# Performance work log

Hardware: AMD Instinct MI355X
Metric: run time of the kernel (lower is better)

## Reference

```python
import jax, jax.numpy as jnp
import numpy as np


def _conv1x1(w, b, x):
    # 1x1 Conv2d == channel matmul: w [O,C], x [B,C,H,W] -> [B,O,H,W]
    return jnp.einsum('oc,bchw->bohw', w, x) + b[None, :, None, None]


def setup_inputs() -> dict:
    key = jax.random.key(0)
    ks = jax.random.split(key, 9)
    C = 512
    B, H, W = 8, 32, 32
    s = 0.02
    return {
        'x': jax.random.normal(ks[0], (B, C, H, W), dtype=jnp.float32),
        'wq': jax.random.normal(ks[1], (C, C), dtype=jnp.float32) * s,
        'bq': jax.random.normal(ks[2], (C,), dtype=jnp.float32) * s,
        'wk': jax.random.normal(ks[3], (C, C), dtype=jnp.float32) * s,
        'bk': jax.random.normal(ks[4], (C,), dtype=jnp.float32) * s,
        'wv': jax.random.normal(ks[5], (C, C), dtype=jnp.float32) * s,
        'bv': jax.random.normal(ks[6], (C,), dtype=jnp.float32) * s,
        'wo': jax.random.normal(ks[7], (C, C), dtype=jnp.float32) * s,
        'bo': jax.random.normal(ks[8], (C,), dtype=jnp.float32) * s,
        'heads': 8,
    }


def reference(x, wq, bq, wk, bk, wv, bv, wo, bo, heads):
    B, C, H, W = x.shape
    N = H * W
    d = C // heads
    scale = jnp.asarray(d, x.dtype) ** 0.5

    vx = _conv1x1(wv, bv, x)                       # value(x), reused for residual
    Q = _conv1x1(wq, bq, x).reshape(B, heads, d, N)
    K = _conv1x1(wk, bk, x).reshape(B, heads, d, N)
    V = vx.reshape(B, heads, d, N)

    attn = jax.nn.softmax(jnp.einsum('bhcn,bhcm->bhnm', Q, K) / scale, axis=-1)
    attn_out = jnp.einsum('bhnm,bhcm->bhcn', attn, V).reshape(B, C, H, W)

    out = attn_out + vx                            # residual uses value(x)
    return _conv1x1(wo, bo, out)
```

## Files before the change

### kernel.cpp

```cpp
#include <hip/hip_runtime.h>
#include <cstdint>
#include <cmath>

#define B_ 8
#define C_ 512
#define N_ 1024
#define H_ 8
#define D_ 64


using u16 = unsigned short;

typedef __bf16 bf16x8 __attribute__((ext_vector_type(8)));
typedef float  f32x4  __attribute__((ext_vector_type(4)));
typedef unsigned short us8 __attribute__((ext_vector_type(8)));


__device__ __forceinline__ float b2f(u16 u) {
    return __uint_as_float(((uint32_t)u) << 16);
}
__device__ __forceinline__ u16 f2b(float f) {
    uint32_t x = __float_as_uint(f);
    return (u16)((x + 0x7fffu + ((x >> 16) & 1u)) >> 16);
}
__device__ __forceinline__ u16 f2bt(float f) {
    return (u16)(__float_as_uint(f) >> 16);
}
__device__ __forceinline__ float sf(float f) {
    return (fabsf(f) < 1e30f) ? f : 0.0f;
}
__device__ __forceinline__ u16 sf2b(float f) { return f2b(sf(f)); }

template<bool WB>
__device__ __forceinline__ us8 ldw(const void* W, size_t idx) {
    if constexpr (WB) {
        return *(const us8*)((const u16*)W + idx);
    } else {
        const float* p = (const float*)W + idx;
        float4 a = *(const float4*)p, b = *(const float4*)(p + 4);
        us8 pk;
        pk[0] = sf2b(a.x); pk[1] = sf2b(a.y); pk[2] = sf2b(a.z); pk[3] = sf2b(a.w);
        pk[4] = sf2b(b.x); pk[5] = sf2b(b.y); pk[6] = sf2b(b.z); pk[7] = sf2b(b.w);
        return pk;
    }
}


__global__ __launch_bounds__(256) void k_wconv(
    const float* __restrict__ wq, const float* __restrict__ wk,
    const float* __restrict__ wv, const float* __restrict__ wo,
    u16* __restrict__ wb) {
    int i = blockIdx.x * 256 + threadIdx.x;
    int m = i >> 16;
    int off = (i & 65535) << 2;
    const float* src = (m == 0) ? wq : (m == 1) ? wk : (m == 2) ? wv : wo;
    float4 v = *(const float4*)&src[off];
    ushort4 w;
    w.x = sf2b(v.x); w.y = sf2b(v.y); w.z = sf2b(v.z); w.w = sf2b(v.w);
    *(ushort4*)&wb[(m << 18) + off] = w;
}


__global__ __launch_bounds__(256) void k_transpose(const float* __restrict__ x,
                                                   u16* __restrict__ xt) {
    __shared__ __align__(16) u16 t[64][72];
    const int tid = threadIdx.x;
    const int nb = blockIdx.x, cb = blockIdx.y, b = blockIdx.z;
#pragma unroll
    for (int i = 0; i < 4; ++i) {
        int q = tid + i * 256;
        int row = q >> 4, cg = q & 15;
        float4 v = *(const float4*)&x[((size_t)(b * C_ + cb * 64 + row) << 10) + nb * 64 + cg * 4];
        ushort4 w;
        w.x = sf2b(v.x); w.y = sf2b(v.y); w.z = sf2b(v.z); w.w = sf2b(v.w);
        *(ushort4*)&t[row][cg * 4] = w;
    }
    __syncthreads();
#pragma unroll
    for (int i = 0; i < 4; ++i) {
        int q = tid + i * 256;
        int nrow = q >> 4, cg = q & 15;
        ushort4 w;
        w.x = t[cg * 4 + 0][nrow];
        w.y = t[cg * 4 + 1][nrow];
        w.z = t[cg * 4 + 2][nrow];
        w.w = t[cg * 4 + 3][nrow];
        *(ushort4*)&xt[((size_t)(b * N_ + nb * 64 + nrow) << 9) + cb * 64 + cg * 4] = w;
    }
}


template<bool WB>
__global__ __launch_bounds__(256) void k_proj_t(
    const u16* __restrict__ xt,
    const void* __restrict__ wq, const float* __restrict__ bq,
    const void* __restrict__ wk, const float* __restrict__ bk,
    const void* __restrict__ wv, const float* __restrict__ bv,
    u16* __restrict__ qt, u16* __restrict__ kt,
    u16* __restrict__ v,  u16* __restrict__ vxt) {
    __shared__ __align__(16) u16 lA[128 * 64];
    __shared__ __align__(16) u16 lB[128 * 64];
    const int tid = threadIdx.x;
    const int op = blockIdx.z >> 3, b = blockIdx.z & 7;
    const int n0 = blockIdx.x * 128, o0 = blockIdx.y * 128;
    const void*  W  = (op == 0) ? wq : (op == 1) ? wk : wv;
    const float* BI = (op == 0) ? bq : (op == 1) ? bk : bv;
    const u16* A = xt + ((size_t)b << 19);
    const int lane = tid & 63, wave = tid >> 6;
    const int wm = (wave >> 1) * 64, wn = (wave & 1) * 64;
    const int l15 = lane & 15, lg = lane >> 4;
    const int xs = (l15 & 7) << 3;

    f32x4 acc[4][4];
    const f32x4 vzero = {0.f, 0.f, 0.f, 0.f};
#pragma unroll
    for (int i = 0; i < 4; ++i)
#pragma unroll
        for (int j = 0; j < 4; ++j) acc[i][j] = vzero;

    us8 ra[4], rwB[4];
    auto loadk = [&](int k0) {
#pragma unroll
        for (int p = 0; p < 4; ++p) {
            int slot = p * 256 + tid;
            int row = slot >> 3, seg = slot & 7;
            ra[p] = *(const us8*)&A[(size_t)(n0 + row) * C_ + k0 + seg * 8];
            rwB[p] = ldw<WB>(W, (size_t)(o0 + row) * C_ + k0 + seg * 8);
        }
    };
    loadk(0);

    for (int k0 = 0; k0 < C_; k0 += 64) {
        __syncthreads();
#pragma unroll
        for (int p = 0; p < 4; ++p) {
            int slot = p * 256 + tid;
            int row = slot >> 3, seg = slot & 7;
            int off = row * 64 + ((seg ^ (row & 7)) << 3);
            *(us8*)&lA[off] = ra[p];
            *(us8*)&lB[off] = rwB[p];
        }
        if (k0 + 64 < C_) loadk(k0 + 64);
        __syncthreads();
#pragma unroll
        for (int kk = 0; kk < 64; kk += 32) {
            const int col = (kk + lg * 8) ^ xs;
            bf16x8 af[4], bfr[4];
#pragma unroll
            for (int i = 0; i < 4; ++i)
                af[i] = *(const bf16x8*)&lA[(wm + i * 16 + l15) * 64 + col];
#pragma unroll
            for (int j = 0; j < 4; ++j)
                bfr[j] = *(const bf16x8*)&lB[(wn + j * 16 + l15) * 64 + col];
#pragma unroll
            for (int i = 0; i < 4; ++i)
#pragma unroll
                for (int j = 0; j < 4; ++j)
                    acc[i][j] = __builtin_amdgcn_mfma_f32_16x16x32_bf16(af[i], bfr[j], acc[i][j], 0, 0, 0);
        }
    }

    if (op < 2) {
        u16* outp = (op == 0) ? qt : kt;
#pragma unroll
        for (int i = 0; i < 4; ++i) {
            int nb2 = n0 + wm + i * 16 + lg * 4;
#pragma unroll
            for (int j = 0; j < 4; ++j) {
                int o = o0 + wn + j * 16 + l15;
                float bias = sf(BI[o]);
                int h = o >> 6, dl = o & 63;
                size_t base = ((size_t)b * H_ + h) << 10;
#pragma unroll
                for (int r = 0; r < 4; ++r)
                    outp[(base + nb2 + r) * D_ + dl] = f2b(acc[i][j][r] + bias);
            }
        }
    } else {
#pragma unroll
        for (int i = 0; i < 4; ++i) {
            int nb2 = n0 + wm + i * 16 + lg * 4;
#pragma unroll
            for (int j = 0; j < 4; ++j) {
                int o = o0 + wn + j * 16 + l15;
                float bias = sf(BI[o]);
                float p0 = acc[i][j][0] + bias, p1 = acc[i][j][1] + bias;
                float p2 = acc[i][j][2] + bias, p3 = acc[i][j][3] + bias;
                ushort4 pk; pk.x = f2b(p0); pk.y = f2b(p1); pk.z = f2b(p2); pk.w = f2b(p3);
                *(ushort4*)&v[((size_t)(b * C_ + o) << 10) + nb2] = pk;
                vxt[((size_t)(b * N_ + nb2 + 0) << 9) + o] = pk.x;
                vxt[((size_t)(b * N_ + nb2 + 1) << 9) + o] = pk.y;
                vxt[((size_t)(b * N_ + nb2 + 2) << 9) + o] = pk.z;
                vxt[((size_t)(b * N_ + nb2 + 3) << 9) + o] = pk.w;
            }
        }
    }
}


__global__ __launch_bounds__(256) void k_attn(
    const u16* __restrict__ qt, const u16* __restrict__ kt,
    const u16* __restrict__ v,  const u16* __restrict__ vxt,
    u16* __restrict__ rt) {
    __shared__ __align__(16) u16 lQ[128 * 64];
    __shared__ __align__(16) u16 lK[128 * 64];
    __shared__ __align__(16) u16 lV[64 * 128];
    __shared__ __align__(16) u16 lP[4][32 * 128];
    const int tid = threadIdx.x, lane = tid & 63, wave = tid >> 6;
    const int l15 = lane & 15, lg = lane >> 4;
    const int xs = (l15 & 7) << 3;
    const int qb = blockIdx.x, bh = blockIdx.y;
    const int b = bh >> 3, h = bh & 7;
    const size_t bh_off = (size_t)bh << 16;
    const int q0 = qb * 128;
    const int nA = wave * 32;

    {
        us8 rq[4];
#pragma unroll
        for (int p = 0; p < 4; ++p) {
            int slot = p * 256 + tid;
            int row = slot >> 3, seg = slot & 7;
            rq[p] = *(const us8*)&qt[bh_off + (size_t)(q0 + row) * D_ + seg * 8];
        }
#pragma unroll
        for (int p = 0; p < 4; ++p) {
            int slot = p * 256 + tid;
            int row = slot >> 3, seg = slot & 7;
            *(us8*)&lQ[row * 64 + ((seg ^ (row & 7)) << 3)] = rq[p];
        }
    }

    us8 rk[4], rv[4];
    auto loadkv = [&](int mb) {
#pragma unroll
        for (int p = 0; p < 4; ++p) {
            int slot = p * 256 + tid;
            int row = slot >> 3, seg = slot & 7;
            rk[p] = *(const us8*)&kt[bh_off + (size_t)(mb * 128 + row) * D_ + seg * 8];
            int vrow = slot >> 4, vseg = slot & 15;
            rv[p] = *(const us8*)&v[((size_t)(b * C_ + h * 64 + vrow) << 10) + mb * 128 + vseg * 8];
        }
    };
    loadkv(0);

    float L[2] = {0.f, 0.f};
    f32x4 oacc[2][4];
    const f32x4 vzero = {0.f, 0.f, 0.f, 0.f};
#pragma unroll
    for (int nt = 0; nt < 2; ++nt)
#pragma unroll
        for (int ct = 0; ct < 4; ++ct) oacc[nt][ct] = vzero;

    for (int mb = 0; mb < 8; ++mb) {
        __syncthreads();
#pragma unroll
        for (int p = 0; p < 4; ++p) {
            int slot = p * 256 + tid;
            int row = slot >> 3, seg = slot & 7;
            *(us8*)&lK[row * 64 + ((seg ^ (row & 7)) << 3)] = rk[p];
            int vrow = slot >> 4, vseg = slot & 15;
            *(us8*)&lV[vrow * 128 + ((vseg ^ (vrow & 7)) << 3)] = rv[p];
        }
        if (mb < 7) loadkv(mb + 1);
        __syncthreads();

        f32x4 s[8][2];
#pragma unroll
        for (int mt = 0; mt < 8; ++mt)
#pragma unroll
            for (int nt = 0; nt < 2; ++nt) s[mt][nt] = vzero;
#pragma unroll
        for (int kk = 0; kk < 64; kk += 32) {
            const int col = (kk + lg * 8) ^ xs;
            bf16x8 aK[8], bQ[2];
#pragma unroll
            for (int mt = 0; mt < 8; ++mt)
                aK[mt] = *(const bf16x8*)&lK[(mt * 16 + l15) * 64 + col];
#pragma unroll
            for (int nt = 0; nt < 2; ++nt)
                bQ[nt] = *(const bf16x8*)&lQ[(nA + nt * 16 + l15) * 64 + col];
            __builtin_amdgcn_s_setprio(1);
#pragma unroll
            for (int mt = 0; mt < 8; ++mt)
#pragma unroll
                for (int nt = 0; nt < 2; ++nt)
                    s[mt][nt] = __builtin_amdgcn_mfma_f32_16x16x32_bf16(aK[mt], bQ[nt], s[mt][nt], 0, 0, 0);
            __builtin_amdgcn_s_setprio(0);
        }

#pragma unroll
        for (int mt = 0; mt < 8; ++mt)
#pragma unroll
            for (int nt = 0; nt < 2; ++nt) {
                float p0 = __expf(s[mt][nt][0] * 0.125f);
                float p1 = __expf(s[mt][nt][1] * 0.125f);
                float p2 = __expf(s[mt][nt][2] * 0.125f);
                float p3 = __expf(s[mt][nt][3] * 0.125f);
                L[nt] += p0 + p1 + p2 + p3;
                ushort4 pk; pk.x = f2bt(p0); pk.y = f2bt(p1); pk.z = f2bt(p2); pk.w = f2bt(p3);
                *(ushort4*)&lP[wave][(nt * 16 + l15) * 128 + ((mt * 16 + lg * 4) ^ xs)] = pk;
            }

#pragma unroll
        for (int kk2 = 0; kk2 < 128; kk2 += 32) {
            const int colv = (kk2 + lg * 8) ^ xs;
            bf16x8 aP[2], bV[4];
#pragma unroll
            for (int nt = 0; nt < 2; ++nt)
                aP[nt] = *(const bf16x8*)&lP[wave][(nt * 16 + l15) * 128 + colv];
#pragma unroll
            for (int ct = 0; ct < 4; ++ct)
                bV[ct] = *(const bf16x8*)&lV[(ct * 16 + l15) * 128 + colv];
            __builtin_amdgcn_s_setprio(1);
#pragma unroll
            for (int nt = 0; nt < 2; ++nt)
#pragma unroll
                for (int ct = 0; ct < 4; ++ct)
                    oacc[nt][ct] = __builtin_amdgcn_mfma_f32_16x16x32_bf16(aP[nt], bV[ct], oacc[nt][ct], 0, 0, 0);
            __builtin_amdgcn_s_setprio(0);
        }
    }

#pragma unroll
    for (int nt = 0; nt < 2; ++nt) {
        float s2 = L[nt];
        s2 += __shfl_xor(s2, 16);
        s2 += __shfl_xor(s2, 32);
        L[nt] = s2;
    }

#pragma unroll
    for (int nt = 0; nt < 2; ++nt) {
        float inv[4];
#pragma unroll
        for (int r = 0; r < 4; ++r) inv[r] = 1.0f / __shfl(L[nt], lg * 4 + r);
#pragma unroll
        for (int ct = 0; ct < 4; ++ct) {
            int ch = h * 64 + ct * 16 + l15;
#pragma unroll
            for (int r = 0; r < 4; ++r) {
                int n = q0 + nA + nt * 16 + lg * 4 + r;
                size_t idx = ((size_t)(b * N_ + n) << 9) + ch;
                rt[idx] = f2b(oacc[nt][ct][r] * inv[r] + b2f(vxt[idx]));
            }
        }
    }
}


template<bool WB>
__global__ __launch_bounds__(256) void k_out_t(
    const u16* __restrict__ rt, const void* __restrict__ wo,
    const float* __restrict__ bo, float* __restrict__ out) {
    __shared__ __align__(16) u16 lA[128 * 64];
    __shared__ __align__(16) u16 lB[128 * 64];
    const int tid = threadIdx.x;
    const int b = blockIdx.z;
    const int n0 = blockIdx.x * 128, o0 = blockIdx.y * 128;
    const u16* Rb = rt + ((size_t)b << 19);
    const int lane = tid & 63, wave = tid >> 6;
    const int wm = (wave >> 1) * 64, wn = (wave & 1) * 64;
    const int l15 = lane & 15, lg = lane >> 4;
    const int xs = (l15 & 7) << 3;

    f32x4 acc[4][4];
    const f32x4 vzero = {0.f, 0.f, 0.f, 0.f};
#pragma unroll
    for (int i = 0; i < 4; ++i)
#pragma unroll
        for (int j = 0; j < 4; ++j) acc[i][j] = vzero;

    us8 rb[4], rwB[4];
    auto loadk = [&](int k0) {
#pragma unroll
        for (int p = 0; p < 4; ++p) {
            int slot = p * 256 + tid;
            int row = slot >> 3, seg = slot & 7;
            rwB[p] = ldw<WB>(wo, (size_t)(o0 + row) * C_ + k0 + seg * 8);
            rb[p] = *(const us8*)&Rb[(size_t)(n0 + row) * C_ + k0 + seg * 8];
        }
    };
    loadk(0);

    for (int k0 = 0; k0 < C_; k0 += 64) {
        __syncthreads();
#pragma unroll
        for (int p = 0; p < 4; ++p) {
            int slot = p * 256 + tid;
            int row = slot >> 3, seg = slot & 7;
            int off = row * 64 + ((seg ^ (row & 7)) << 3);
            *(us8*)&lA[off] = rwB[p];
            *(us8*)&lB[off] = rb[p];
        }
        if (k0 + 64 < C_) loadk(k0 + 64);
        __syncthreads();
#pragma unroll
        for (int kk = 0; kk < 64; kk += 32) {
            const int col = (kk + lg * 8) ^ xs;
            bf16x8 af[4], bfr[4];
#pragma unroll
            for (int i = 0; i < 4; ++i)
                af[i] = *(const bf16x8*)&lA[(wm + i * 16 + l15) * 64 + col];
#pragma unroll
            for (int j = 0; j < 4; ++j)
                bfr[j] = *(const bf16x8*)&lB[(wn + j * 16 + l15) * 64 + col];
#pragma unroll
            for (int i = 0; i < 4; ++i)
#pragma unroll
                for (int j = 0; j < 4; ++j)
                    acc[i][j] = __builtin_amdgcn_mfma_f32_16x16x32_bf16(af[i], bfr[j], acc[i][j], 0, 0, 0);
        }
    }

#pragma unroll
    for (int i = 0; i < 4; ++i) {
#pragma unroll
        for (int j = 0; j < 4; ++j) {
            int nn = n0 + wn + j * 16 + l15;
#pragma unroll
            for (int r = 0; r < 4; ++r) {
                int o = o0 + wm + i * 16 + lg * 4 + r;
                out[((size_t)(b * C_ + o) << 10) + nn] = acc[i][j][r] + sf(bo[o]);
            }
        }
    }
}


extern "C" void kernel_launch(void* const* d_in, const int* in_sizes, int n_in,
                              void* d_out, int out_size, void* d_ws, size_t ws_size,
                              hipStream_t stream) {
    const float* x  = (const float*)d_in[0];
    const float* wq = (const float*)d_in[1];
    const float* bq = (const float*)d_in[2];
    const float* wk = (const float*)d_in[3];
    const float* bk = (const float*)d_in[4];
    const float* wv = (const float*)d_in[5];
    const float* bv = (const float*)d_in[6];
    const float* wo = (const float*)d_in[7];
    const float* bo = (const float*)d_in[8];
    float* out = (float*)d_out;
    u16* ws = (u16*)d_ws;

    const size_t T = (size_t)B_ * C_ * N_;
    const size_t WSZ = (size_t)4 * C_ * C_;
    if (ws_size < 5 * T * sizeof(u16)) return;

    u16* xt  = ws;
    u16* qt  = ws + 1 * T;
    u16* kt  = ws + 2 * T;
    u16* vv  = ws + 3 * T;
    u16* vxt = ws + 4 * T;
    u16* rt  = xt;
    u16* wb  = ws + 5 * T;

    const bool wbfit = ws_size >= (5 * T + WSZ) * sizeof(u16);

    k_transpose<<<dim3(16, 8, 8), 256, 0, stream>>>(x, xt);
    if (wbfit) {
        k_wconv<<<dim3(1024), 256, 0, stream>>>(wq, wk, wv, wo, wb);
        k_proj_t<true><<<dim3(8, 4, 24), 256, 0, stream>>>(
            xt, wb, bq, wb + 262144, bk, wb + 524288, bv, qt, kt, vv, vxt);
    } else {
        k_proj_t<false><<<dim3(8, 4, 24), 256, 0, stream>>>(
            xt, wq, bq, wk, bk, wv, bv, qt, kt, vv, vxt);
    }
    k_attn<<<dim3(8, 64), 256, 0, stream>>>(qt, kt, vv, vxt, rt);
    if (wbfit) {
        k_out_t<true><<<dim3(8, 4, 8), 256, 0, stream>>>(rt, wb + 786432, bo, out);
    } else {
        k_out_t<false><<<dim3(8, 4, 8), 256, 0, stream>>>(rt, wo, bo, out);
    }
}
```

Baseline: 87.59 us.

## Keep Q in registers, halve KV tile, fold softmax scale into Q projection

The attention kernel now loads Q fragments straight into registers instead of staging them through shared memory. It processes keys and values in 64-wide tiles (16 iterations) instead of 128, which roughly halves shared memory use and should allow more resident blocks. The softmax scale and log2(e) are folded into the Q projection epilogue so the kernel can use a hardware exp2 without a multiply. The grid is flattened to 1D with head-major block ordering. The trade-off is twice as many barriers per block and extra bf16 rounding of the pre-scaled Q.

```diff
diff --git a/kernel.cpp b/kernel.cpp
--- a/kernel.cpp
+++ b/kernel.cpp
@@ -14,6 +14,14 @@
 typedef __bf16 bf16x8 __attribute__((ext_vector_type(8)));
 typedef float  f32x4  __attribute__((ext_vector_type(4)));
 typedef unsigned short us8 __attribute__((ext_vector_type(8)));
+
+#if __has_builtin(__builtin_amdgcn_exp2f)
+#define EXP2(x) __builtin_amdgcn_exp2f(x)
+#else
+#define EXP2(x) exp2f(x)
+#endif
+
+#define QSCALE 0.1803368801111244f
 
 
 __device__ __forceinline__ float b2f(u16 u) {
@@ -162,6 +170,7 @@
 
     if (op < 2) {
         u16* outp = (op == 0) ? qt : kt;
+        const float scl = (op == 0) ? QSCALE : 1.0f;
 #pragma unroll
         for (int i = 0; i < 4; ++i) {
             int nb2 = n0 + wm + i * 16 + lg * 4;
@@ -173,7 +182,7 @@
                 size_t base = ((size_t)b * H_ + h) << 10;
 #pragma unroll
                 for (int r = 0; r < 4; ++r)
-                    outp[(base + nb2 + r) * D_ + dl] = f2b(acc[i][j][r] + bias);
+                    outp[(base + nb2 + r) * D_ + dl] = f2b((acc[i][j][r] + bias) * scl);
             }
         }
     } else {
@@ -202,44 +211,35 @@
     const u16* __restrict__ qt, const u16* __restrict__ kt,
     const u16* __restrict__ v,  const u16* __restrict__ vxt,
     u16* __restrict__ rt) {
-    __shared__ __align__(16) u16 lQ[128 * 64];
-    __shared__ __align__(16) u16 lK[128 * 64];
-    __shared__ __align__(16) u16 lV[64 * 128];
-    __shared__ __align__(16) u16 lP[4][32 * 128];
+    __shared__ __align__(16) u16 lK[64 * 64];
+    __shared__ __align__(16) u16 lV[64 * 64];
+    __shared__ __align__(16) u16 lP[4][32 * 64];
     const int tid = threadIdx.x, lane = tid & 63, wave = tid >> 6;
     const int l15 = lane & 15, lg = lane >> 4;
     const int xs = (l15 & 7) << 3;
-    const int qb = blockIdx.x, bh = blockIdx.y;
+    const int bid = blockIdx.x;
+    const int qb = bid >> 6, bh = bid & 63;
     const int b = bh >> 3, h = bh & 7;
     const size_t bh_off = (size_t)bh << 16;
     const int q0 = qb * 128;
     const int nA = wave * 32;
 
-    {
-        us8 rq[4];
-#pragma unroll
-        for (int p = 0; p < 4; ++p) {
-            int slot = p * 256 + tid;
-            int row = slot >> 3, seg = slot & 7;
-            rq[p] = *(const us8*)&qt[bh_off + (size_t)(q0 + row) * D_ + seg * 8];
-        }
-#pragma unroll
-        for (int p = 0; p < 4; ++p) {
-            int slot = p * 256 + tid;
-            int row = slot >> 3, seg = slot & 7;
-            *(us8*)&lQ[row * 64 + ((seg ^ (row & 7)) << 3)] = rq[p];
-        }
-    }
-
-    us8 rk[4], rv[4];
+    bf16x8 qf[2][2];
+#pragma unroll
+    for (int nt = 0; nt < 2; ++nt)
+#pragma unroll
+        for (int k = 0; k < 2; ++k)
+            qf[nt][k] = *(const bf16x8*)&qt[bh_off +
+                (size_t)(q0 + nA + nt * 16 + l15) * D_ + k * 32 + lg * 8];
+
+    us8 rk[2], rv[2];
     auto loadkv = [&](int mb) {
 #pragma unroll
-        for (int p = 0; p < 4; ++p) {
-            int slot = p * 256 + tid;
-            int row = slot >> 3, seg = slot & 7;
-            rk[p] = *(const us8*)&kt[bh_off + (size_t)(mb * 128 + row) * D_ + seg * 8];
-            int vrow = slot >> 4, vseg = slot & 15;
-            rv[p] = *(const us8*)&v[((size_t)(b * C_ + h * 64 + vrow) << 10) + mb * 128 + vseg * 8];
+        for (int p = 0; p < 2; ++p) {
+            int slot = p * 256 + tid;
+            int row = slot >> 3, seg = slot & 7;
+            rk[p] = *(const us8*)&kt[bh_off + (size_t)(mb * 64 + row) * D_ + seg * 8];
+            rv[p] = *(const us8*)&v[((size_t)(b * C_ + h * 64 + row) << 10) + mb * 64 + seg * 8];
         }
     };
     loadkv(0);
@@ -252,66 +252,63 @@
 #pragma unroll
         for (int ct = 0; ct < 4; ++ct) oacc[nt][ct] = vzero;
 
-    for (int mb = 0; mb < 8; ++mb) {
-        __syncthreads();
-#pragma unroll
-        for (int p = 0; p < 4; ++p) {
-            int slot = p * 256 + tid;
-            int row = slot >> 3, seg = slot & 7;
-            *(us8*)&lK[row * 64 + ((seg ^ (row & 7)) << 3)] = rk[p];
-            int vrow = slot >> 4, vseg = slot & 15;
-            *(us8*)&lV[vrow * 128 + ((vseg ^ (vrow & 7)) << 3)] = rv[p];
-        }
-        if (mb < 7) loadkv(mb + 1);
-        __syncthreads();
-
-        f32x4 s[8][2];
-#pragma unroll
-        for (int mt = 0; mt < 8; ++mt)
+    for (int mb = 0; mb < 16; ++mb) {
+        __syncthreads();
+#pragma unroll
+        for (int p = 0; p < 2; ++p) {
+            int slot = p * 256 + tid;
+            int row = slot >> 3, seg = slot & 7;
+            int off = row * 64 + ((seg ^ (row & 7)) << 3);
+            *(us8*)&lK[off] = rk[p];
+            *(us8*)&lV[off] = rv[p];
+        }
+        if (mb < 15) loadkv(mb + 1);
+        __syncthreads();
+
+        f32x4 s[4][2];
+#pragma unroll
+        for (int mt = 0; mt < 4; ++mt)
 #pragma unroll
             for (int nt = 0; nt < 2; ++nt) s[mt][nt] = vzero;
 #pragma unroll
-        for (int kk = 0; kk < 64; kk += 32) {
-            const int col = (kk + lg * 8) ^ xs;
-            bf16x8 aK[8], bQ[2];
-#pragma unroll
-            for (int mt = 0; mt < 8; ++mt)
+        for (int k = 0; k < 2; ++k) {
+            const int col = (k * 32 + lg * 8) ^ xs;
+            bf16x8 aK[4];
+#pragma unroll
+            for (int mt = 0; mt < 4; ++mt)
                 aK[mt] = *(const bf16x8*)&lK[(mt * 16 + l15) * 64 + col];
-#pragma unroll
-            for (int nt = 0; nt < 2; ++nt)
-                bQ[nt] = *(const bf16x8*)&lQ[(nA + nt * 16 + l15) * 64 + col];
             __builtin_amdgcn_s_setprio(1);
 #pragma unroll
-            for (int mt = 0; mt < 8; ++mt)
+            for (int mt = 0; mt < 4; ++mt)
 #pragma unroll
                 for (int nt = 0; nt < 2; ++nt)
-                    s[mt][nt] = __builtin_amdgcn_mfma_f32_16x16x32_bf16(aK[mt], bQ[nt], s[mt][nt], 0, 0, 0);
+                    s[mt][nt] = __builtin_amdgcn_mfma_f32_16x16x32_bf16(aK[mt], qf[nt][k], s[mt][nt], 0, 0, 0);
             __builtin_amdgcn_s_setprio(0);
         }
 
 #pragma unroll
-        for (int mt = 0; mt < 8; ++mt)
+        for (int mt = 0; mt < 4; ++mt)
 #pragma unroll
             for (int nt = 0; nt < 2; ++nt) {
-                float p0 = __expf(s[mt][nt][0] * 0.125f);
-                float p1 = __expf(s[mt][nt][1] * 0.125f);
-                float p2 = __expf(s[mt][nt][2] * 0.125f);
-                float p3 = __expf(s[mt][nt][3] * 0.125f);
+                float p0 = EXP2(s[mt][nt][0]);
+                float p1 = EXP2(s[mt][nt][1]);
+                float p2 = EXP2(s[mt][nt][2]);
+                float p3 = EXP2(s[mt][nt][3]);
                 L[nt] += p0 + p1 + p2 + p3;
                 ushort4 pk; pk.x = f2bt(p0); pk.y = f2bt(p1); pk.z = f2bt(p2); pk.w = f2bt(p3);
-                *(ushort4*)&lP[wave][(nt * 16 + l15) * 128 + ((mt * 16 + lg * 4) ^ xs)] = pk;
+                *(ushort4*)&lP[wave][(nt * 16 + l15) * 64 + ((mt * 16 + lg * 4) ^ xs)] = pk;
             }
 
 #pragma unroll
-        for (int kk2 = 0; kk2 < 128; kk2 += 32) {
+        for (int kk2 = 0; kk2 < 64; kk2 += 32) {
             const int colv = (kk2 + lg * 8) ^ xs;
             bf16x8 aP[2], bV[4];
 #pragma unroll
             for (int nt = 0; nt < 2; ++nt)
-                aP[nt] = *(const bf16x8*)&lP[wave][(nt * 16 + l15) * 128 + colv];
+                aP[nt] = *(const bf16x8*)&lP[wave][(nt * 16 + l15) * 64 + colv];
 #pragma unroll
             for (int ct = 0; ct < 4; ++ct)
-                bV[ct] = *(const bf16x8*)&lV[(ct * 16 + l15) * 128 + colv];
+                bV[ct] = *(const bf16x8*)&lV[(ct * 16 + l15) * 64 + colv];
             __builtin_amdgcn_s_setprio(1);
 #pragma unroll
             for (int nt = 0; nt < 2; ++nt)
@@ -466,7 +463,7 @@
         k_proj_t<false><<<dim3(8, 4, 24), 256, 0, stream>>>(
             xt, wq, bq, wk, bk, wv, bv, qt, kt, vv, vxt);
     }
-    k_attn<<<dim3(8, 64), 256, 0, stream>>>(qt, kt, vv, vxt, rt);
+    k_attn<<<dim3(512), 256, 0, stream>>>(qt, kt, vv, vxt, rt);
     if (wbfit) {
         k_out_t<true><<<dim3(8, 4, 8), 256, 0, stream>>>(rt, wb + 786432, bo, out);
     } else {
```

Measured after the change: 76.04 us. -13.2%, faster.
